# Performance work log

Measured on AMD Instinct MI355X. Metric: run time of the kernel, lower is better.

## Reference

```python
import jax, jax.numpy as jnp
import numpy as np

TEMPERATURE = 0.07
MASK_VAL = -9e15
EPS = 1e-8

def setup_inputs() -> dict:
    key = jax.random.key(0)
    features = jax.random.normal(key, (8192, 256), dtype=jnp.float32)
    return {"features": features}

def reference(features):
    # features: [N, D]
    N = features.shape[0]
    norm = jnp.linalg.norm(features, axis=-1, keepdims=True)
    f = features / jnp.maximum(norm, EPS)
    # cosine similarity via GEMM: [N, N]
    sim = f @ f.T
    idx = jnp.arange(N)
    # mask self-similarity BEFORE temperature scaling (as in the torch code)
    sim = jnp.where(idx[:, None] == idx[None, :], MASK_VAL, sim)
    sim = sim / TEMPERATURE
    # positive of row i is column (i - N//2) mod N (eye rolled by N//2 along dim 0)
    pos_col = (idx - N // 2) % N
    pos = sim[idx, pos_col]
    nll = -pos + jax.nn.logsumexp(sim, axis=-1)
    return nll.mean()
```

## Files before the change

kernel.cpp:

```cpp
#include <hip/hip_runtime.h>
#include <hip/hip_bf16.h>
#include <math.h>

#define N_ROWS 8192
#define D_DIM  256
#define HALF_N 4096
#define NBLK   512
#define INV_T      14.285714285714286f
#define SCALE_LOG2 20.609929155556620f
#define NEG_SCALE  -20.609929155556620f
#define EPSV   1e-8f

typedef __attribute__((ext_vector_type(8))) short bf16x8;
typedef __attribute__((ext_vector_type(4))) float f32x4;

#define AS1 __attribute__((address_space(1)))
#define AS3 __attribute__((address_space(3)))
#define AGT __HIP_MEMORY_SCOPE_AGENT

__device__ unsigned g_done = 0;

__device__ inline unsigned short f2bf(float x) {
    unsigned int u = __float_as_uint(x);
    unsigned int r = (u + 0x7fffu + ((u >> 16) & 1u)) >> 16;
    return (unsigned short)r;
}

__global__ __launch_bounds__(256) void k_prep(const float* __restrict__ feat,
                                              unsigned short* __restrict__ fbf,
                                              float* __restrict__ sumexp,
                                              float* __restrict__ posv) {
    const int tid = threadIdx.x, w = tid >> 6, lane = tid & 63;
    const int row = blockIdx.x * 4 + w;
    const int pc  = (row + HALF_N) & (N_ROWS - 1);

    const float4 v = ((const float4*)(feat + row * D_DIM))[lane];
    const float4 c = ((const float4*)(feat + pc  * D_DIM))[lane];
    float ss  = v.x*v.x + v.y*v.y + v.z*v.z + v.w*v.w;
    float dab = v.x*c.x + v.y*c.y + v.z*c.z + v.w*c.w;
    float dbb = c.x*c.x + c.y*c.y + c.z*c.z + c.w*c.w;
    #pragma unroll
    for (int off = 32; off; off >>= 1) {
        ss  += __shfl_xor(ss,  off);
        dab += __shfl_xor(dab, off);
        dbb += __shfl_xor(dbb, off);
    }
    const float na = fmaxf(sqrtf(ss), EPSV);
    const float sc = 1.f / na;
    ushort4 o;
    o.x = f2bf(v.x * sc); o.y = f2bf(v.y * sc);
    o.z = f2bf(v.z * sc); o.w = f2bf(v.w * sc);
    ((ushort4*)(fbf + row * D_DIM))[lane] = o;
    if (lane == 0)
        posv[row] = INV_T - (dab / (na * fmaxf(sqrtf(dbb), EPSV))) * INV_T;
    if (tid < 4) sumexp[blockIdx.x * 4 + tid] = 0.f;
}

__global__ __launch_bounds__(256, 2) void k_simfin(const unsigned short* __restrict__ fbf,
                                                   float* __restrict__ sumexp,
                                                   const float* __restrict__ posv,
                                                   float* __restrict__ out) {
    __shared__ __align__(16) char Bs[16384];
    __shared__ float red[4];
    __shared__ int lastBlk;
    const int tid  = threadIdx.x;
    const int lane = tid & 63;
    const int w    = tid >> 6;
    const int q    = lane >> 4, l15 = lane & 15;

    int g          = (33 * blockIdx.x) >> 2;
    const int gEnd = (33 * (blockIdx.x + 1)) >> 2;

    const int tt0 = g >> 3;
    int rt = (int)((sqrtf(8.f * (float)tt0 + 1.f) - 1.f) * 0.5f);
    while ((rt + 1) * (rt + 2) / 2 <= tt0) ++rt;
    while (rt * (rt + 1) / 2 > tt0) --rt;
    int cs = tt0 - rt * (rt + 1) / 2;
    int jt = g & 7;

#define STAGE(colRow0) do {                                                   \
        const char* Bg_ = (const char*)fbf + (size_t)(colRow0) * 512;         \
        _Pragma("unroll")                                                     \
        for (int i_ = 0; i_ < 4; ++i_) {                                      \
            const int idx_ = i_ * 256 + tid;                                  \
            const int col_ = idx_ >> 5;                                       \
            const int cir_ = idx_ & 31;                                       \
            __builtin_amdgcn_global_load_lds(                                 \
                (const AS1 void*)(Bg_ + col_ * 512 + ((cir_ ^ (col_ & 7)) << 4)), \
                (AS3 void*)(Bs + idx_ * 16), 16, 0, 0);                       \
        }                                                                     \
    } while (0)

    bf16x8 afrag[8][4];
#define LOAD_A(rt_) do {                                                      \
        const int rowBase_ = (rt_) * 256 + w * 64;                            \
        _Pragma("unroll")                                                     \
        for (int t_ = 0; t_ < 8; ++t_)                                        \
            _Pragma("unroll")                                                 \
            for (int ri_ = 0; ri_ < 4; ++ri_)                                 \
                afrag[t_][ri_] = *(const bf16x8*)(fbf                         \
                    + (rowBase_ + ri_*16 + l15) * D_DIM + t_*32 + q*8);       \
    } while (0)

    float rsum[4][4];
#define ZERO_RSUM() do {                                                      \
        _Pragma("unroll")                                                     \
        for (int ri_ = 0; ri_ < 4; ++ri_)                                     \
            _Pragma("unroll")                                                 \
            for (int r_ = 0; r_ < 4; ++r_) rsum[ri_][r_] = 0.f;               \
    } while (0)

#define FLUSH_RSUM(rt_) do {                                                  \
        const int rowBase_ = (rt_) * 256 + w * 64;                            \
        _Pragma("unroll")                                                     \
        for (int ri_ = 0; ri_ < 4; ++ri_)                                     \
            _Pragma("unroll")                                                 \
            for (int r_ = 0; r_ < 4; ++r_) {                                  \
                float s_ = rsum[ri_][r_];                                     \
                s_ += __shfl_xor(s_, 1);                                      \
                s_ += __shfl_xor(s_, 2);                                      \
                s_ += __shfl_xor(s_, 4);                                      \
                s_ += __shfl_xor(s_, 8);                                      \
                if (l15 == 0)                                                 \
                    atomicAdd(&sumexp[rowBase_ + ri_ * 16 + q * 4 + r_], s_); \
            }                                                                 \
    } while (0)

    STAGE(cs * 256 + jt * 32);
    LOAD_A(rt);
    ZERO_RSUM();

    while (true) {
        const int colBase = cs * 256 + jt * 32;
        const bool isDiag = (rt == cs);
        const int rowBase = rt * 256 + w * 64;

        __syncthreads();

        f32x4 acc[4][2];
        #pragma unroll
        for (int ri = 0; ri < 4; ++ri)
            #pragma unroll
            for (int ci = 0; ci < 2; ++ci) acc[ri][ci] = (f32x4){0.f, 0.f, 0.f, 0.f};

        #pragma unroll
        for (int t = 0; t < 8; ++t) {
            bf16x8 bfrag[2];
            #pragma unroll
            for (int ci = 0; ci < 2; ++ci) {
                const int c   = ci * 16 + l15;
                const int cir = t * 4 + q;
                bfrag[ci] = *(const bf16x8*)(Bs + c * 512 + ((cir ^ (c & 7)) << 4));
            }
            #pragma unroll
            for (int ri = 0; ri < 4; ++ri)
                #pragma unroll
                for (int ci = 0; ci < 2; ++ci)
                    acc[ri][ci] = __builtin_amdgcn_mfma_f32_16x16x32_bf16(
                        afrag[t][ri], bfrag[ci], acc[ri][ci], 0, 0, 0);
        }

        const bool more = (g + 1 < gEnd);
        int nrt = rt, ncs = cs, njt = jt + 1;
        if (njt == 8) {
            njt = 0; ncs = cs + 1;
            if (ncs > rt) { nrt = rt + 1; ncs = 0; }
        }

        if (more) {
            __syncthreads();
            STAGE(ncs * 256 + njt * 32);
            if (njt == 0) LOAD_A(nrt);
        }

        if (isDiag) {
            #pragma unroll
            for (int ri = 0; ri < 4; ++ri) {
                const int trow = rowBase + ri * 16;
                #pragma unroll
                for (int ci = 0; ci < 2; ++ci) {
                    const int tcol = colBase + ci * 16;
                    if (trow == tcol) {
                        #pragma unroll
                        for (int r = 0; r < 4; ++r) {
                            const float e = __builtin_amdgcn_exp2f(
                                __builtin_fmaf(acc[ri][ci][r], SCALE_LOG2, NEG_SCALE));
                            rsum[ri][r] += (q * 4 + r == l15) ? 0.f : e;
                        }
                    } else {
                        #pragma unroll
                        for (int r = 0; r < 4; ++r)
                            rsum[ri][r] += __builtin_amdgcn_exp2f(
                                __builtin_fmaf(acc[ri][ci][r], SCALE_LOG2, NEG_SCALE));
                    }
                }
            }
        } else {
            float csum0 = 0.f, csum1 = 0.f;
            #pragma unroll
            for (int ri = 0; ri < 4; ++ri) {
                #pragma unroll
                for (int r = 0; r < 4; ++r) {
                    const float e0 = __builtin_amdgcn_exp2f(
                        __builtin_fmaf(acc[ri][0][r], SCALE_LOG2, NEG_SCALE));
                    const float e1 = __builtin_amdgcn_exp2f(
                        __builtin_fmaf(acc[ri][1][r], SCALE_LOG2, NEG_SCALE));
                    rsum[ri][r] += e0 + e1;
                    csum0 += e0;
                    csum1 += e1;
                }
            }
            csum0 += __shfl_xor(csum0, 16); csum0 += __shfl_xor(csum0, 32);
            csum1 += __shfl_xor(csum1, 16); csum1 += __shfl_xor(csum1, 32);
            if (q == 0)      atomicAdd(&sumexp[colBase      + l15], csum0);
            else if (q == 1) atomicAdd(&sumexp[colBase + 16 + l15], csum1);
        }

        if (!more) break;
        if (njt == 0) {
            FLUSH_RSUM(rt);
            ZERO_RSUM();
        }
        rt = nrt; cs = ncs; jt = njt; ++g;
    }

    FLUSH_RSUM(rt);
#undef STAGE
#undef LOAD_A
#undef ZERO_RSUM
#undef FLUSH_RSUM

    __syncthreads();
    if (tid == 0) {
        const unsigned old = __hip_atomic_fetch_add(&g_done, 1u, __ATOMIC_ACQ_REL, AGT);
        lastBlk = ((old & (NBLK - 1)) == NBLK - 1);
    }
    __syncthreads();
    if (lastBlk) {
        float wsum = 0.f;
        for (int i = tid; i < N_ROWS; i += 256)
            wsum += posv[i] + logf(sumexp[i]);
        #pragma unroll
        for (int off = 32; off; off >>= 1) wsum += __shfl_xor(wsum, off);
        if (lane == 0) red[w] = wsum;
        __syncthreads();
        if (tid == 0)
            out[0] = (red[0] + red[1] + red[2] + red[3]) * (1.f / N_ROWS);
    }
}

extern "C" void kernel_launch(void* const* d_in, const int* in_sizes, int n_in,
                              void* d_out, int out_size, void* d_ws, size_t ws_size,
                              hipStream_t stream) {
    const float* feat = (const float*)d_in[0];
    char* ws = (char*)d_ws;
    unsigned short* fbf = (unsigned short*)ws;
    float* sumexp = (float*)(ws + 4u * 1024u * 1024u);
    float* posv   = (float*)(ws + 4u * 1024u * 1024u + 32768u);

    k_prep  <<<N_ROWS / 4, 256, 0, stream>>>(feat, fbf, sumexp, posv);
    k_simfin<<<NBLK,       256, 0, stream>>>(fbf, sumexp, posv, (float*)d_out);
}
```

Before: 108.1 us.

## Assign one full tile per block plus split-column blocks for the tail tiles

The balanced work split, where each of 512 blocks walked about 8.25 column-chunks across tile boundaries, is replaced by a static mapping onto 640 blocks. The first 512 blocks each handle one complete 256x256 upper-triangle tile (8 column chunks). The remaining 16 tiles are split into 128 single-chunk blocks. This removes the mid-loop A reloads and row-sum flushes, but the 128 tail blocks each do far less work than the rest, and the grid size and completion-counter modulus change to match.

```diff
diff --git a/kernel.cpp b/kernel.cpp
--- a/kernel.cpp
+++ b/kernel.cpp
@@ -5,7 +5,7 @@
 #define N_ROWS 8192
 #define D_DIM  256
 #define HALF_N 4096
-#define NBLK   512
+#define NBLK   640u
 #define INV_T      14.285714285714286f
 #define SCALE_LOG2 20.609929155556620f
 #define NEG_SCALE  -20.609929155556620f
@@ -67,16 +67,18 @@
     const int lane = tid & 63;
     const int w    = tid >> 6;
     const int q    = lane >> 4, l15 = lane & 15;
-
-    int g          = (33 * blockIdx.x) >> 2;
-    const int gEnd = (33 * (blockIdx.x + 1)) >> 2;
-
-    const int tt0 = g >> 3;
-    int rt = (int)((sqrtf(8.f * (float)tt0 + 1.f) - 1.f) * 0.5f);
-    while ((rt + 1) * (rt + 2) / 2 <= tt0) ++rt;
-    while (rt * (rt + 1) / 2 > tt0) --rt;
-    int cs = tt0 - rt * (rt + 1) / 2;
-    int jt = g & 7;
+    const int b    = blockIdx.x;
+
+    int tt, jtBegin, jtEnd;
+    if (b < 512) { tt = b;                      jtBegin = 0;            jtEnd = 8; }
+    else         { tt = 512 + ((b - 512) >> 3); jtBegin = (b - 512) & 7; jtEnd = jtBegin + 1; }
+
+    int rt = (int)((sqrtf(8.f * (float)tt + 1.f) - 1.f) * 0.5f);
+    while ((rt + 1) * (rt + 2) / 2 <= tt) ++rt;
+    while (rt * (rt + 1) / 2 > tt) --rt;
+    const int cs = tt - rt * (rt + 1) / 2;
+    const bool isDiag = (rt == cs);
+    const int rowBase = rt * 256 + w * 64;
 
 #define STAGE(colRow0) do {                                                   \
         const char* Bg_ = (const char*)fbf + (size_t)(colRow0) * 512;         \
@@ -92,48 +94,23 @@
     } while (0)
 
     bf16x8 afrag[8][4];
-#define LOAD_A(rt_) do {                                                      \
-        const int rowBase_ = (rt_) * 256 + w * 64;                            \
-        _Pragma("unroll")                                                     \
-        for (int t_ = 0; t_ < 8; ++t_)                                        \
-            _Pragma("unroll")                                                 \
-            for (int ri_ = 0; ri_ < 4; ++ri_)                                 \
-                afrag[t_][ri_] = *(const bf16x8*)(fbf                         \
-                    + (rowBase_ + ri_*16 + l15) * D_DIM + t_*32 + q*8);       \
-    } while (0)
+    #pragma unroll
+    for (int t = 0; t < 8; ++t)
+        #pragma unroll
+        for (int ri = 0; ri < 4; ++ri)
+            afrag[t][ri] = *(const bf16x8*)(fbf + (rowBase + ri*16 + l15) * D_DIM
+                                                + t*32 + q*8);
 
     float rsum[4][4];
-#define ZERO_RSUM() do {                                                      \
-        _Pragma("unroll")                                                     \
-        for (int ri_ = 0; ri_ < 4; ++ri_)                                     \
-            _Pragma("unroll")                                                 \
-            for (int r_ = 0; r_ < 4; ++r_) rsum[ri_][r_] = 0.f;               \
-    } while (0)
-
-#define FLUSH_RSUM(rt_) do {                                                  \
-        const int rowBase_ = (rt_) * 256 + w * 64;                            \
-        _Pragma("unroll")                                                     \
-        for (int ri_ = 0; ri_ < 4; ++ri_)                                     \
-            _Pragma("unroll")                                                 \
-            for (int r_ = 0; r_ < 4; ++r_) {                                  \
-                float s_ = rsum[ri_][r_];                                     \
-                s_ += __shfl_xor(s_, 1);                                      \
-                s_ += __shfl_xor(s_, 2);                                      \
-                s_ += __shfl_xor(s_, 4);                                      \
-                s_ += __shfl_xor(s_, 8);                                      \
-                if (l15 == 0)                                                 \
-                    atomicAdd(&sumexp[rowBase_ + ri_ * 16 + q * 4 + r_], s_); \
-            }                                                                 \
-    } while (0)
-
-    STAGE(cs * 256 + jt * 32);
-    LOAD_A(rt);
-    ZERO_RSUM();
-
-    while (true) {
+    #pragma unroll
+    for (int ri = 0; ri < 4; ++ri)
+        #pragma unroll
+        for (int r = 0; r < 4; ++r) rsum[ri][r] = 0.f;
+
+    STAGE(cs * 256 + jtBegin * 32);
+
+    for (int jt = jtBegin; jt < jtEnd; ++jt) {
         const int colBase = cs * 256 + jt * 32;
-        const bool isDiag = (rt == cs);
-        const int rowBase = rt * 256 + w * 64;
 
         __syncthreads();
 
@@ -160,17 +137,9 @@
                         afrag[t][ri], bfrag[ci], acc[ri][ci], 0, 0, 0);
         }
 
-        const bool more = (g + 1 < gEnd);
-        int nrt = rt, ncs = cs, njt = jt + 1;
-        if (njt == 8) {
-            njt = 0; ncs = cs + 1;
-            if (ncs > rt) { nrt = rt + 1; ncs = 0; }
-        }
-
-        if (more) {
+        if (jt + 1 < jtEnd) {
             __syncthreads();
-            STAGE(ncs * 256 + njt * 32);
-            if (njt == 0) LOAD_A(nrt);
+            STAGE(cs * 256 + (jt + 1) * 32);
         }
 
         if (isDiag) {
@@ -215,25 +184,26 @@
             if (q == 0)      atomicAdd(&sumexp[colBase      + l15], csum0);
             else if (q == 1) atomicAdd(&sumexp[colBase + 16 + l15], csum1);
         }
-
-        if (!more) break;
-        if (njt == 0) {
-            FLUSH_RSUM(rt);
-            ZERO_RSUM();
-        }
-        rt = nrt; cs = ncs; jt = njt; ++g;
-    }
-
-    FLUSH_RSUM(rt);
+    }
+
+    #pragma unroll
+    for (int ri = 0; ri < 4; ++ri)
+        #pragma unroll
+        for (int r = 0; r < 4; ++r) {
+            float s = rsum[ri][r];
+            s += __shfl_xor(s, 1);
+            s += __shfl_xor(s, 2);
+            s += __shfl_xor(s, 4);
+            s += __shfl_xor(s, 8);
+            if (l15 == 0)
+                atomicAdd(&sumexp[rowBase + ri * 16 + q * 4 + r], s);
+        }
 #undef STAGE
-#undef LOAD_A
-#undef ZERO_RSUM
-#undef FLUSH_RSUM
 
     __syncthreads();
     if (tid == 0) {
         const unsigned old = __hip_atomic_fetch_add(&g_done, 1u, __ATOMIC_ACQ_REL, AGT);
-        lastBlk = ((old & (NBLK - 1)) == NBLK - 1);
+        lastBlk = ((old % NBLK) == NBLK - 1u);
     }
     __syncthreads();
     if (lastBlk) {
```

Result: slower. 115.3 us (+6.7%).
